# Kernel tuning notes

Hardware: AMD Instinct MI355X
Metric: run time of the kernel (lower is better)

Reference implementation:

```python
import jax, jax.numpy as jnp
import numpy as np

BATCH, NATOMS, NBONDS, NSPEC = 50, 512, 4096, 2


def _taper(r, rmin, rmax):
    # taper() from the source (bond-order cutoff smoothing)
    r3 = jnp.where(r > rmax, 1.0, 0.0)
    ok = (r <= rmax) & (r > rmin)
    r2 = jnp.where(ok, r, 0.0)
    r20 = jnp.where(ok, 1.0, 0.0)
    rterm = 1.0 / (rmin - rmax) ** 3
    rm = rmin * r20
    rd = rm - r2
    trm1 = rm + 2.0 * r2 - 3.0 * rmax * r20
    return rterm * rd * rd * trm1 + r3


def _fnn(xs, wi, w, b, wo, bo):
    # tiny sigmoid MLP fnn(): xs [B,NB,3] -> [B,NB]
    o = jax.nn.sigmoid(xs @ wi)              # [B,NB,8]
    for l in range(w.shape[0]):
        o = jax.nn.sigmoid(o @ w[l] + b[l])  # [B,NB,8]
    return jax.nn.sigmoid(o @ wo + bo)[..., 0]


def _forward(x, cell, rcell, sp_p, gp, bp, fe_wi, fe_w, fe_b, fe_wo, fe_bo, bdid, spec):
    lp1, ovun3, ovun4, ovun6, ovun7, ovun8, botol = (gp[i] for i in range(7))
    rosi, ropi, ropp, bo1, bo2, bo3, bo4, bo5, bo6, Desi = (bp[i] for i in range(10))
    B, N = x.shape[0], x.shape[1]
    # fvr + minimum image: vr[b,i,j] = x[b,i] - x[b,j]
    vr = x[:, :, None, :] - x[:, None, :, :]          # [B,N,N,3]
    vrf = jnp.einsum('bijk,bkl->bijl', vr, rcell)
    vrf = jnp.where(vrf > 0.5, vrf - 1.0, vrf)
    vrf = jnp.where(vrf < -0.5, vrf + 1.0, vrf)
    vr = jnp.einsum('bijk,bkl->bijl', vrf, cell)
    r = jnp.sqrt(jnp.sum(vr * vr, axis=3))            # [B,N,N]

    i0, i1 = bdid[:, 0], bdid[:, 1]
    rbd = r[:, i0, i1]                                # gather bonded pairs [B,NB]
    # uncorrected bond orders (get_bondorder_uc)
    eterm1 = (1.0 + botol) * jnp.exp(bo1 * (rbd / rosi) ** bo2)
    eterm2 = jnp.exp(bo3 * (rbd / ropi) ** bo4)
    eterm3 = jnp.exp(bo5 * (rbd / ropp) ** bo6)
    bop_si_v = _taper(eterm1, botol, 2.0 * botol) * (eterm1 - botol)
    bop_pi_v = _taper(eterm2, botol, 2.0 * botol) * eterm2
    bop_pp_v = _taper(eterm3, botol, 2.0 * botol) * eterm3

    def sym(v):  # symmetric scatter into dense [B,N,N]
        z = jnp.zeros((B, N, N), v.dtype)
        return z.at[:, i0, i1].set(v).at[:, i1, i0].set(v)

    bop_si = sym(bop_si_v)
    bop_pi = sym(bop_pi_v)
    bop_pp = sym(bop_pp_v)
    bop = bop_si + bop_pi + bop_pp
    Delta = jnp.sum(bop, axis=2)                      # [B,N]
    Delta_pi = jnp.sum(bop_pi + bop_pp, axis=2)
    SO = jnp.sum(bop_si, axis=2)

    # bond energy: fnn on (bosi,bopi,bopp), ebond = sum over scattered ebd matrix
    xs = jnp.stack([bop_si_v, bop_pi_v, bop_pp_v], axis=2)  # [B,NB,3]
    esi = _fnn(xs, fe_wi, fe_w, fe_b, fe_wo, fe_bo)
    ebond = jnp.sum(-Desi * esi, axis=1)              # [B]

    # per-species gather of atomic params (vectorized species loop)
    pa = sp_p[spec]                                   # [N,5]
    val, vale, lp2, ovun2, ovun5 = pa[:, 0], pa[:, 1], pa[:, 2], pa[:, 3], pa[:, 4]

    # get_elone
    Nlp = 0.5 * (vale - val)
    delta_e = 0.5 * (Delta - vale)
    De = -jax.nn.relu(-jnp.ceil(delta_e))
    nlp = -De + jnp.exp(-lp1 * 4.0 * jnp.square(1.0 + delta_e - De))
    Delta_lp = jax.nn.relu(Nlp - nlp + 1.0) - 1.0
    Elone = lp2 * Delta_lp / (1.0 + jnp.exp(-75.0 * Delta_lp))

    # get_eover
    dlpcorr = Delta - val - Delta_lp / (1.0 + ovun3 * jnp.exp(ovun4 * Delta_pi))
    denom = dlpcorr + val
    otrm1 = 1.0 / jnp.where(denom != 0.0, denom, 1e-8)  # DIV_IF
    Eover = SO * otrm1 * dlpcorr * jax.nn.sigmoid(-ovun2 * dlpcorr)

    # get_eunder
    Eunder = (-ovun5 * (1.0 - jnp.exp(ovun6 * dlpcorr)) * jax.nn.sigmoid(ovun2 * dlpcorr)
              / (1.0 + ovun7 * jnp.exp(ovun8 * Delta_pi)))

    return ebond + jnp.sum(Elone + Eover + Eunder, axis=1)  # total energy per frame [B]


def setup_inputs() -> dict:
    key = jax.random.key(0)
    ks = jax.random.split(key, 8)
    L = 20.0  # cubic cell edge (Angstrom)
    x = jax.random.uniform(ks[0], (BATCH, NATOMS, 3), dtype=jnp.float32) * L
    cell = jnp.tile(jnp.eye(3, dtype=jnp.float32) * L, (BATCH, 1, 1))
    rcell = jnp.tile(jnp.eye(3, dtype=jnp.float32) / L, (BATCH, 1, 1))
    rng = np.random.default_rng(0)
    i0 = rng.integers(0, NATOMS, NBONDS)
    j0 = (i0 + rng.integers(1, NATOMS, NBONDS)) % NATOMS
    bdid = jnp.asarray(np.stack([np.minimum(i0, j0), np.maximum(i0, j0)], 1), dtype=jnp.int32)
    spec = jax.random.randint(ks[1], (NATOMS,), 0, NSPEC, dtype=jnp.int32)
    # [val, vale, lp2, ovun2, ovun5] per species
    sp_p = jnp.array([[4.0, 4.0, 0.1, -4.0, 30.0],
                      [2.0, 6.0, 15.0, -4.0, 30.0]], jnp.float32)
    # [lp1, ovun3, ovun4, ovun6, ovun7, ovun8, botol]
    gp = jnp.array([18.0, 3.0, 5.0, 8.0, 11.0, 13.0, 0.01], jnp.float32)
    # [rosi, ropi, ropp, bo1, bo2, bo3, bo4, bo5, bo6, Desi]
    bp = jnp.array([1.4, 1.2, 1.1, -0.08, 6.0, -0.1, 7.0, -0.2, 8.0, 120.0], jnp.float32)
    fe_wi = jax.random.normal(ks[2], (3, 8), jnp.float32)
    fe_w = jax.random.normal(ks[3], (5, 8, 8), jnp.float32) * 0.5
    fe_b = jax.random.normal(ks[4], (5, 8), jnp.float32) * 0.1
    fe_wo = jax.random.normal(ks[5], (8, 1), jnp.float32)
    fe_bo = jax.random.normal(ks[6], (1,), jnp.float32) * 0.1
    return dict(x=x, cell=cell, rcell=rcell, sp_p=sp_p, gp=gp, bp=bp,
                fe_wi=fe_wi, fe_w=fe_w, fe_b=fe_b, fe_wo=fe_wo, fe_bo=fe_bo,
                bdid=bdid, spec=spec)


def reference(x, cell, rcell, sp_p, gp, bp, fe_wi, fe_w, fe_b, fe_wo, fe_bo, bdid, spec):
    return _forward(x, cell, rcell, sp_p, gp, bp, fe_wi, fe_w, fe_b, fe_wo, fe_bo, bdid, spec)
```

## Files before the change

### kernel.cpp

```cpp
#include <hip/hip_runtime.h>

#define BATCH 50
#define NATOMS 512
#define NBONDS 4096
#define NXF (NATOMS*3)
#define ILP 2
#define BPB (NBONDS/(256*ILP))
#define BITS_W (NATOMS*NATOMS/32)

__device__ __forceinline__ float sigmoidf_(float x){ return 1.f/(1.f+__expf(-x)); }

__device__ __forceinline__ float taperf_(float r, float rmin, float rmax){
    float r3  = (r > rmax) ? 1.f : 0.f;
    bool  ok  = (r <= rmax) && (r > rmin);
    float r2  = ok ? r   : 0.f;
    float r20 = ok ? 1.f : 0.f;
    float d   = rmin - rmax;
    float rterm = 1.f/(d*d*d);
    float rm  = rmin*r20;
    float rd  = rm - r2;
    float trm1 = rm + 2.f*r2 - 3.f*rmax*r20;
    return rterm*rd*rd*trm1 + r3;
}

__global__ __launch_bounds__(256) void claim_kernel(const int* __restrict__ bdid,
                                                    unsigned* __restrict__ bits,
                                                    float* __restrict__ ownerf){
    int k = blockIdx.x*256 + threadIdx.x;
    int2 ij = ((const int2*)bdid)[k];
    unsigned pidx = (unsigned)(ij.x*NATOMS + ij.y);
    unsigned old = atomicOr(&bits[pidx>>5], 1u<<(pidx&31));
    ownerf[k] = ((old>>(pidx&31)) & 1u) ? 0.f : 1.f;
}

__global__ __launch_bounds__(256) void fused_kernel(
    const float* __restrict__ x, const float* __restrict__ cell, const float* __restrict__ rcell,
    const float* __restrict__ sp_p, const float* __restrict__ gp, const float* __restrict__ bp,
    const float* __restrict__ fe_wi, const float* __restrict__ fe_w, const float* __restrict__ fe_b,
    const float* __restrict__ fe_wo, const float* __restrict__ fe_bo,
    const int* __restrict__ bdid, const int* __restrict__ spec,
    const float* __restrict__ ownerf,
    float* __restrict__ Delta, float* __restrict__ Delta_pi, float* __restrict__ SO,
    float* __restrict__ ebond_acc, unsigned* __restrict__ done,
    float* __restrict__ out)
{
    __shared__ float s_x[NXF];
    __shared__ float accD[NATOMS], accP[NATOMS], accS[NATOMS];
    __shared__ __align__(16) float s_w[320];
    __shared__ __align__(16) float s_wo[8];
    __shared__ float s_wi[24], s_bb[40];
    __shared__ float s_part[4];
    __shared__ unsigned s_rank;
    int tid = threadIdx.x;
    int b   = blockIdx.y;

    const float4* xb4 = (const float4*)(x + (size_t)b*NXF);
    float4* sx4 = (float4*)s_x;
    sx4[tid] = xb4[tid];
    if(tid < NXF/4 - 256) sx4[tid+256] = xb4[tid+256];
    for(int n=tid; n<NATOMS; n+=256){ accD[n]=0.f; accP[n]=0.f; accS[n]=0.f; }
    for(int t=tid; t<320; t+=256){
        int l = t>>6, rr = t&63, v = rr>>3, u = rr&7;
        s_w[(l<<6) + (u<<3) + v] = fe_w[t];
    }
    if(tid < 24) s_wi[tid] = fe_wi[tid];
    if(tid < 40) s_bb[tid] = fe_b[tid];
    if(tid < 8)  s_wo[tid] = fe_wo[tid];
    __syncthreads();

    float botol = gp[6];
    float rosi=bp[0], ropi=bp[1], ropp=bp[2];
    float bo1=bp[3], bo2=bp[4], bo3=bp[5], bo4=bp[6], bo5=bp[7], bo6=bp[8], Desi=bp[9];
    float bo_out = fe_bo[0];
    const float* cb = cell  + b*9;
    const float* rb = rcell + b*9;
    float tmax = 2.f*botol;

    int kbase = blockIdx.x*(256*ILP) + tid;
    float o[ILP][8];

    #pragma unroll
    for(int q=0;q<ILP;q++){
        int k = kbase + q*256;
        float own = ownerf[k];
        int2 ij = ((const int2*)bdid)[k];
        int i = ij.x, j = ij.y;
        float dx0 = s_x[3*i+0]-s_x[3*j+0];
        float dx1 = s_x[3*i+1]-s_x[3*j+1];
        float dx2 = s_x[3*i+2]-s_x[3*j+2];
        float f0 = dx0*rb[0]+dx1*rb[3]+dx2*rb[6];
        float f1 = dx0*rb[1]+dx1*rb[4]+dx2*rb[7];
        float f2 = dx0*rb[2]+dx1*rb[5]+dx2*rb[8];
        f0 = (f0>0.5f)?f0-1.f:f0; f0 = (f0<-0.5f)?f0+1.f:f0;
        f1 = (f1>0.5f)?f1-1.f:f1; f1 = (f1<-0.5f)?f1+1.f:f1;
        f2 = (f2>0.5f)?f2-1.f:f2; f2 = (f2<-0.5f)?f2+1.f:f2;
        float v0 = f0*cb[0]+f1*cb[3]+f2*cb[6];
        float v1 = f0*cb[1]+f1*cb[4]+f2*cb[7];
        float v2 = f0*cb[2]+f1*cb[5]+f2*cb[8];
        float r = sqrtf(v0*v0+v1*v1+v2*v2);

        float eterm1 = (1.f+botol)*__expf(bo1*__powf(r/rosi, bo2));
        float eterm2 = __expf(bo3*__powf(r/ropi, bo4));
        float eterm3 = __expf(bo5*__powf(r/ropp, bo6));
        float si = taperf_(eterm1, botol, tmax)*(eterm1-botol);
        float pi = taperf_(eterm2, botol, tmax)*eterm2;
        float pp = taperf_(eterm3, botol, tmax)*eterm3;

        float bop = own*(si+pi+pp), dpi = own*(pi+pp), osi = own*si;
        atomicAdd(&accD[i], bop); atomicAdd(&accD[j], bop);
        atomicAdd(&accP[i], dpi); atomicAdd(&accP[j], dpi);
        atomicAdd(&accS[i], osi); atomicAdd(&accS[j], osi);

        #pragma unroll
        for(int u=0;u<8;u++)
            o[q][u] = sigmoidf_(si*s_wi[u] + pi*s_wi[8+u] + pp*s_wi[16+u]);
    }

    #pragma unroll
    for(int l=0;l<5;l++){
        const float4* wl = (const float4*)(s_w + (l<<6));
        const float*  bl = s_bb + (l<<3);
        float no[ILP][8];
        #pragma unroll
        for(int u=0;u<8;u++){
            float4 wa = wl[2*u], wb = wl[2*u+1];
            #pragma unroll
            for(int q=0;q<ILP;q++){
                float a0 = fmaf(o[q][0],wa.x, bl[u]);
                float a1 = o[q][1]*wa.y;
                a0 = fmaf(o[q][2],wa.z,a0); a1 = fmaf(o[q][3],wa.w,a1);
                a0 = fmaf(o[q][4],wb.x,a0); a1 = fmaf(o[q][5],wb.y,a1);
                a0 = fmaf(o[q][6],wb.z,a0); a1 = fmaf(o[q][7],wb.w,a1);
                no[q][u] = sigmoidf_(a0+a1);
            }
        }
        #pragma unroll
        for(int q=0;q<ILP;q++)
            #pragma unroll
            for(int u=0;u<8;u++) o[q][u]=no[q][u];
    }
    float4 woa = ((const float4*)s_wo)[0], wob = ((const float4*)s_wo)[1];
    float esum = 0.f;
    #pragma unroll
    for(int q=0;q<ILP;q++){
        float a0 = fmaf(o[q][0],woa.x, bo_out);
        float a1 = o[q][1]*woa.y;
        a0 = fmaf(o[q][2],woa.z,a0); a1 = fmaf(o[q][3],woa.w,a1);
        a0 = fmaf(o[q][4],wob.x,a0); a1 = fmaf(o[q][5],wob.y,a1);
        a0 = fmaf(o[q][6],wob.z,a0); a1 = fmaf(o[q][7],wob.w,a1);
        esum += sigmoidf_(a0+a1);
    }

    float ev = -Desi*esum;
    #pragma unroll
    for(int o2=32;o2>0;o2>>=1) ev += __shfl_down(ev, o2, 64);
    if((tid & 63) == 0) s_part[tid>>6] = ev;
    __syncthreads();
    if(tid==0) atomicAdd(&ebond_acc[b], s_part[0]+s_part[1]+s_part[2]+s_part[3]);

    float* Db = Delta    + (size_t)b*NATOMS;
    float* Pb = Delta_pi + (size_t)b*NATOMS;
    float* Sb = SO       + (size_t)b*NATOMS;
    for(int n=tid; n<NATOMS; n+=256){
        atomicAdd(&Db[n], accD[n]);
        atomicAdd(&Pb[n], accP[n]);
        atomicAdd(&Sb[n], accS[n]);
    }

    __syncthreads();
    if(tid==0) s_rank = atomicAdd(&done[b], 1u);
    __syncthreads();
    if(s_rank != BPB-1) return;

    float lp1=gp[0], ovun3=gp[1], ovun4=gp[2], ovun6=gp[3], ovun7=gp[4], ovun8=gp[5];
    float acc = 0.f;
    for(int n=tid; n<NATOMS; n+=256){
        int s = spec[n];
        const float* pa = sp_p + s*5;
        float val=pa[0], vale=pa[1], lp2=pa[2], ovun2=pa[3], ovun5=pa[4];
        size_t idx = (size_t)b*NATOMS + n;
        float D   = __hip_atomic_load(&Delta[idx],    __ATOMIC_RELAXED, __HIP_MEMORY_SCOPE_AGENT);
        float Dpi = __hip_atomic_load(&Delta_pi[idx], __ATOMIC_RELAXED, __HIP_MEMORY_SCOPE_AGENT);
        float so  = __hip_atomic_load(&SO[idx],       __ATOMIC_RELAXED, __HIP_MEMORY_SCOPE_AGENT);

        float Nlp = 0.5f*(vale-val);
        float de  = 0.5f*(D-vale);
        float De  = fminf(ceilf(de), 0.f);
        float t   = 1.f + de - De;
        float nlp = -De + __expf(-lp1*4.f*t*t);
        float Dlp = fmaxf(Nlp - nlp + 1.f, 0.f) - 1.f;
        float Elone = lp2*Dlp/(1.f+__expf(-75.f*Dlp));
        float dlp = D - val - Dlp/(1.f + ovun3*__expf(ovun4*Dpi));
        float denom = dlp + val;
        float otrm1 = 1.f/((denom!=0.f)?denom:1e-8f);
        float Eover = so*otrm1*dlp*sigmoidf_(-ovun2*dlp);
        float Eunder = -ovun5*(1.f-__expf(ovun6*dlp))*sigmoidf_(ovun2*dlp)
                       /(1.f + ovun7*__expf(ovun8*Dpi));
        acc += Elone + Eover + Eunder;
    }
    #pragma unroll
    for(int o2=32;o2>0;o2>>=1) acc += __shfl_down(acc, o2, 64);
    __syncthreads();
    if((tid & 63) == 0) s_part[tid>>6] = acc;
    __syncthreads();
    if(tid==0){
        float eb = __hip_atomic_load(&ebond_acc[b], __ATOMIC_RELAXED, __HIP_MEMORY_SCOPE_AGENT);
        out[b] = eb + s_part[0]+s_part[1]+s_part[2]+s_part[3];
    }
}

extern "C" void kernel_launch(void* const* d_in, const int* in_sizes, int n_in,
                              void* d_out, int out_size, void* d_ws, size_t ws_size,
                              hipStream_t stream)
{
    const float* x     = (const float*)d_in[0];
    const float* cell  = (const float*)d_in[1];
    const float* rcell = (const float*)d_in[2];
    const float* sp_p  = (const float*)d_in[3];
    const float* gp    = (const float*)d_in[4];
    const float* bp    = (const float*)d_in[5];
    const float* fe_wi = (const float*)d_in[6];
    const float* fe_w  = (const float*)d_in[7];
    const float* fe_b  = (const float*)d_in[8];
    const float* fe_wo = (const float*)d_in[9];
    const float* fe_bo = (const float*)d_in[10];
    const int*   bdid  = (const int*)d_in[11];
    const int*   spec  = (const int*)d_in[12];
    float* out = (float*)d_out;

    float* Delta     = (float*)d_ws;
    float* Delta_pi  = Delta + BATCH*NATOMS;
    float* SO        = Delta_pi + BATCH*NATOMS;
    float* ebond_acc = SO + BATCH*NATOMS;
    unsigned* done   = (unsigned*)(ebond_acc + BATCH);
    unsigned* bits   = done + BATCH;
    float* ownerf    = (float*)(bits + BITS_W);

    size_t zbytes = (size_t)(3*BATCH*NATOMS + BATCH)*sizeof(float)
                  + (size_t)BATCH*sizeof(unsigned)
                  + (size_t)BITS_W*sizeof(unsigned);
    hipMemsetAsync(d_ws, 0, zbytes, stream);
    hipMemsetAsync(out, 0, BATCH*sizeof(float), stream);

    claim_kernel<<<dim3(NBONDS/256), 256, 0, stream>>>(bdid, bits, ownerf);
    fused_kernel<<<dim3(BPB, BATCH), 256, 0, stream>>>(
        x, cell, rcell, sp_p, gp, bp, fe_wi, fe_w, fe_b, fe_wo, fe_bo,
        bdid, spec, ownerf, Delta, Delta_pi, SO, ebond_acc, done, out);
}
```

Before: 111.9 us.

## Replace global atomics and memsets with per-block partial buffers and shared-memory claim bitmap

Each block now writes its per-atom partial sums and its bond-energy partial to its own slice of the workspace, and the last block per batch sums those slices. This replaces the per-element global atomicAdds and removes both hipMemsetAsync calls. The claim kernel becomes a single 1024-thread block that keeps its dedup bitmap in shared memory and resets the done counters itself. The aim is to cut launch and memset overhead and atomic contention, at the cost of a serial single-block claim pass and a wider final reduction.

```diff
diff --git a/kernel.cpp b/kernel.cpp
--- a/kernel.cpp
+++ b/kernel.cpp
@@ -23,14 +23,20 @@
     return rterm*rd*rd*trm1 + r3;
 }
 
-__global__ __launch_bounds__(256) void claim_kernel(const int* __restrict__ bdid,
-                                                    unsigned* __restrict__ bits,
-                                                    float* __restrict__ ownerf){
-    int k = blockIdx.x*256 + threadIdx.x;
-    int2 ij = ((const int2*)bdid)[k];
-    unsigned pidx = (unsigned)(ij.x*NATOMS + ij.y);
-    unsigned old = atomicOr(&bits[pidx>>5], 1u<<(pidx&31));
-    ownerf[k] = ((old>>(pidx&31)) & 1u) ? 0.f : 1.f;
+__global__ __launch_bounds__(1024) void claim_kernel(const int* __restrict__ bdid,
+                                                     float* __restrict__ ownerf,
+                                                     unsigned* __restrict__ done){
+    __shared__ unsigned bits[BITS_W];
+    int tid = threadIdx.x;
+    for(int t=tid; t<BITS_W; t+=1024) bits[t] = 0u;
+    if(tid < BATCH) done[tid] = 0u;
+    __syncthreads();
+    for(int k=tid; k<NBONDS; k+=1024){
+        int2 ij = ((const int2*)bdid)[k];
+        unsigned pidx = (unsigned)(ij.x*NATOMS + ij.y);
+        unsigned old = atomicOr(&bits[pidx>>5], 1u<<(pidx&31));
+        ownerf[k] = ((old>>(pidx&31)) & 1u) ? 0.f : 1.f;
+    }
 }
 
 __global__ __launch_bounds__(256) void fused_kernel(
@@ -40,8 +46,8 @@
     const float* __restrict__ fe_wo, const float* __restrict__ fe_bo,
     const int* __restrict__ bdid, const int* __restrict__ spec,
     const float* __restrict__ ownerf,
-    float* __restrict__ Delta, float* __restrict__ Delta_pi, float* __restrict__ SO,
-    float* __restrict__ ebond_acc, unsigned* __restrict__ done,
+    float* __restrict__ Dpart, float* __restrict__ Ppart, float* __restrict__ Spart,
+    float* __restrict__ epart, unsigned* __restrict__ done,
     float* __restrict__ out)
 {
     __shared__ float s_x[NXF];
@@ -156,16 +162,17 @@
     for(int o2=32;o2>0;o2>>=1) ev += __shfl_down(ev, o2, 64);
     if((tid & 63) == 0) s_part[tid>>6] = ev;
     __syncthreads();
-    if(tid==0) atomicAdd(&ebond_acc[b], s_part[0]+s_part[1]+s_part[2]+s_part[3]);
-
-    float* Db = Delta    + (size_t)b*NATOMS;
-    float* Pb = Delta_pi + (size_t)b*NATOMS;
-    float* Sb = SO       + (size_t)b*NATOMS;
+
+    size_t sl = ((size_t)b*BPB + blockIdx.x)*NATOMS;
     for(int n=tid; n<NATOMS; n+=256){
-        atomicAdd(&Db[n], accD[n]);
-        atomicAdd(&Pb[n], accP[n]);
-        atomicAdd(&Sb[n], accS[n]);
-    }
+        __hip_atomic_store(&Dpart[sl+n], accD[n], __ATOMIC_RELAXED, __HIP_MEMORY_SCOPE_AGENT);
+        __hip_atomic_store(&Ppart[sl+n], accP[n], __ATOMIC_RELAXED, __HIP_MEMORY_SCOPE_AGENT);
+        __hip_atomic_store(&Spart[sl+n], accS[n], __ATOMIC_RELAXED, __HIP_MEMORY_SCOPE_AGENT);
+    }
+    if(tid==0)
+        __hip_atomic_store(&epart[b*BPB + blockIdx.x],
+                           s_part[0]+s_part[1]+s_part[2]+s_part[3],
+                           __ATOMIC_RELAXED, __HIP_MEMORY_SCOPE_AGENT);
 
     __syncthreads();
     if(tid==0) s_rank = atomicAdd(&done[b], 1u);
@@ -175,13 +182,18 @@
     float lp1=gp[0], ovun3=gp[1], ovun4=gp[2], ovun6=gp[3], ovun7=gp[4], ovun8=gp[5];
     float acc = 0.f;
     for(int n=tid; n<NATOMS; n+=256){
+        float D=0.f, Dpi=0.f, so=0.f;
+        size_t base = (size_t)b*BPB*NATOMS + n;
+        #pragma unroll
+        for(int blk=0; blk<BPB; blk++){
+            size_t idx = base + (size_t)blk*NATOMS;
+            D   += __hip_atomic_load(&Dpart[idx], __ATOMIC_RELAXED, __HIP_MEMORY_SCOPE_AGENT);
+            Dpi += __hip_atomic_load(&Ppart[idx], __ATOMIC_RELAXED, __HIP_MEMORY_SCOPE_AGENT);
+            so  += __hip_atomic_load(&Spart[idx], __ATOMIC_RELAXED, __HIP_MEMORY_SCOPE_AGENT);
+        }
         int s = spec[n];
         const float* pa = sp_p + s*5;
         float val=pa[0], vale=pa[1], lp2=pa[2], ovun2=pa[3], ovun5=pa[4];
-        size_t idx = (size_t)b*NATOMS + n;
-        float D   = __hip_atomic_load(&Delta[idx],    __ATOMIC_RELAXED, __HIP_MEMORY_SCOPE_AGENT);
-        float Dpi = __hip_atomic_load(&Delta_pi[idx], __ATOMIC_RELAXED, __HIP_MEMORY_SCOPE_AGENT);
-        float so  = __hip_atomic_load(&SO[idx],       __ATOMIC_RELAXED, __HIP_MEMORY_SCOPE_AGENT);
 
         float Nlp = 0.5f*(vale-val);
         float de  = 0.5f*(D-vale);
@@ -204,7 +216,10 @@
     if((tid & 63) == 0) s_part[tid>>6] = acc;
     __syncthreads();
     if(tid==0){
-        float eb = __hip_atomic_load(&ebond_acc[b], __ATOMIC_RELAXED, __HIP_MEMORY_SCOPE_AGENT);
+        float eb = 0.f;
+        #pragma unroll
+        for(int blk=0; blk<BPB; blk++)
+            eb += __hip_atomic_load(&epart[b*BPB + blk], __ATOMIC_RELAXED, __HIP_MEMORY_SCOPE_AGENT);
         out[b] = eb + s_part[0]+s_part[1]+s_part[2]+s_part[3];
     }
 }
@@ -228,22 +243,15 @@
     const int*   spec  = (const int*)d_in[12];
     float* out = (float*)d_out;
 
-    float* Delta     = (float*)d_ws;
-    float* Delta_pi  = Delta + BATCH*NATOMS;
-    float* SO        = Delta_pi + BATCH*NATOMS;
-    float* ebond_acc = SO + BATCH*NATOMS;
-    unsigned* done   = (unsigned*)(ebond_acc + BATCH);
-    unsigned* bits   = done + BATCH;
-    float* ownerf    = (float*)(bits + BITS_W);
-
-    size_t zbytes = (size_t)(3*BATCH*NATOMS + BATCH)*sizeof(float)
-                  + (size_t)BATCH*sizeof(unsigned)
-                  + (size_t)BITS_W*sizeof(unsigned);
-    hipMemsetAsync(d_ws, 0, zbytes, stream);
-    hipMemsetAsync(out, 0, BATCH*sizeof(float), stream);
-
-    claim_kernel<<<dim3(NBONDS/256), 256, 0, stream>>>(bdid, bits, ownerf);
+    float* Dpart  = (float*)d_ws;
+    float* Ppart  = Dpart + (size_t)BATCH*BPB*NATOMS;
+    float* Spart  = Ppart + (size_t)BATCH*BPB*NATOMS;
+    float* epart  = Spart + (size_t)BATCH*BPB*NATOMS;
+    unsigned* done = (unsigned*)(epart + BATCH*BPB);
+    float* ownerf  = (float*)(done + BATCH);
+
+    claim_kernel<<<dim3(1), 1024, 0, stream>>>(bdid, ownerf, done);
     fused_kernel<<<dim3(BPB, BATCH), 256, 0, stream>>>(
         x, cell, rcell, sp_p, gp, bp, fe_wi, fe_w, fe_b, fe_wo, fe_bo,
-        bdid, spec, ownerf, Delta, Delta_pi, SO, ebond_acc, done, out);
-}
+        bdid, spec, ownerf, Dpart, Ppart, Spart, epart, done, out);
+}
```

Measured after the change: 110.9 us. About the same (-0.9%).
